# Optimization experiments

Hardware: AMD Instinct MI355X
Metric: run time of the kernel (lower is better)

## Reference

```python
import jax, jax.numpy as jnp
import numpy as np

N = 50000    # nodes
E = 600000   # edges
F = 128      # num_features
ED = 16      # edge_dim
H = 4        # heads
D = 32       # per-head channels = hidden_units // heads
HID = H * D  # hidden_units = 128
C = 10       # num_classes


def _lin(k, fan_in, fan_out):
    # torch.nn.Linear-style init scale
    return jax.random.uniform(k, (fan_in, fan_out), jnp.float32, -1.0, 1.0) / np.sqrt(fan_in)


def setup_inputs() -> dict:
    key = jax.random.key(0)
    ks = jax.random.split(key, 24)
    inp = {
        "x": jax.random.normal(ks[0], (N, F), jnp.float32),
        "edge_index": jax.random.randint(ks[1], (2, E), 0, N, dtype=jnp.int32),
        "edge_attr": jax.random.normal(ks[2], (E, ED), jnp.float32),
    }
    j = 3
    for l, ind in enumerate([F, HID]):
        specs = {"q": (ind, HID, True), "k": (ind, HID, True), "v": (ind, HID, True),
                 "e": (ED, HID, False), "s": (ind, HID, True)}
        for nm, (i, o, bias) in specs.items():
            inp[f"W{nm}{l}"] = _lin(ks[j], i, o); j += 1
            if bias:
                inp[f"b{nm}{l}"] = jnp.zeros((o,), jnp.float32)
    inp["Wout"] = _lin(ks[j], HID, C)
    inp["bout"] = jnp.zeros((C,), jnp.float32)
    return inp


def _transformer_conv(x, src, dst, eattr, Wq, bq, Wk, bk, Wv, bv, We, Ws, bs):
    # PyG TransformerConv: concat=True, root_weight=True, beta=False, eval dropout.
    n = x.shape[0]
    q = (x @ Wq + bq).reshape(n, H, D)
    k = (x @ Wk + bk).reshape(n, H, D)
    v = (x @ Wv + bv).reshape(n, H, D)
    e = (eattr @ We).reshape(-1, H, D)           # edge embedding, added to key and value
    kj = k[src] + e                              # [E, H, D]
    vj = v[src] + e                              # [E, H, D]
    logits = jnp.einsum("ehd,ehd->eh", q[dst], kj) / np.sqrt(D)
    m = jax.ops.segment_max(logits, dst, num_segments=n)          # [N, H]
    ex = jnp.exp(logits - m[dst])
    denom = jax.ops.segment_sum(ex, dst, num_segments=n)          # [N, H]
    alpha = ex / (denom[dst] + 1e-16)                             # PyG softmax eps
    out = jax.ops.segment_sum(vj * alpha[..., None], dst, num_segments=n)
    return out.reshape(n, HID) + x @ Ws + bs                      # concat heads + skip


def reference(x, edge_index, edge_attr,
              Wq0, bq0, Wk0, bk0, Wv0, bv0, We0, Ws0, bs0,
              Wq1, bq1, Wk1, bk1, Wv1, bv1, We1, Ws1, bs1,
              Wout, bout):
    src, dst = edge_index[0], edge_index[1]
    h = jax.nn.relu(_transformer_conv(x, src, dst, edge_attr,
                                      Wq0, bq0, Wk0, bk0, Wv0, bv0, We0, Ws0, bs0))
    h = jax.nn.relu(_transformer_conv(h, src, dst, edge_attr,
                                      Wq1, bq1, Wk1, bk1, Wv1, bv1, We1, Ws1, bs1))
    logits = h @ Wout + bout
    return jax.nn.log_softmax(logits, axis=1)
```

## Files before the change

kernel.cpp:

```cpp
#include <hip/hip_runtime.h>

typedef unsigned short u16;
typedef unsigned int u32;
typedef __attribute__((ext_vector_type(4))) u16 u16x4;
typedef __attribute__((ext_vector_type(8))) u16 u16x8;
typedef __attribute__((ext_vector_type(4))) u32 u32x4;
typedef __attribute__((ext_vector_type(8))) short short8;
typedef __attribute__((ext_vector_type(4))) float f32x4;
typedef __attribute__((ext_vector_type(4))) float f4;
typedef __attribute__((ext_vector_type(2))) float f2;

#define NN 50000
#define NE 600000
#define HEADS 4
#define DH 32
#define HIDU 128
#define NC 10
#define NBLK 196
#define WES_T 34
#define WES_H 546

#define SCALE2 0.25503486164f

__device__ __forceinline__ float bf2f(u16 u) {
    union { unsigned int i; float f; } c; c.i = ((unsigned int)u) << 16; return c.f;
}
__device__ __forceinline__ u16 f2bf(float f) {
    union { float f; unsigned int i; } c; c.f = f;
    unsigned int x = c.i;
    return (u16)((x + 0x7fffu + ((x >> 16) & 1u)) >> 16);
}
__device__ __forceinline__ float lo_bf(u32 d) { return __uint_as_float(d << 16); }
__device__ __forceinline__ float hi_bf(u32 d) { return __uint_as_float(d & 0xffff0000u); }
__device__ __forceinline__ float qadd_xor1(float v) {
    int o = __builtin_amdgcn_update_dpp(0, __float_as_int(v), 0xB1, 0xF, 0xF, true);
    return v + __int_as_float(o);
}
__device__ __forceinline__ float qadd_xor2(float v) {
    int o = __builtin_amdgcn_update_dpp(0, __float_as_int(v), 0x4E, 0xF, 0xF, true);
    return v + __int_as_float(o);
}

__global__ void k_zero(int* p, int n) {
    int i = blockIdx.x * blockDim.x + threadIdx.x;
    if (i < n) p[i] = 0;
}

__global__ void k_hist(const int* __restrict__ dst, int* __restrict__ deg) {
    int i = blockIdx.x * blockDim.x + threadIdx.x;
    if (i < NE) atomicAdd(&deg[dst[i]], 1);
}

__global__ __launch_bounds__(256) void scan_a(const int* __restrict__ deg,
                                              int* __restrict__ bsum) {
    __shared__ int red[4];
    int i = blockIdx.x * 256 + threadIdx.x;
    int v = (i < NN) ? deg[i] : 0;
    #pragma unroll
    for (int off = 1; off < 64; off <<= 1) v += __shfl_xor(v, off);
    if ((threadIdx.x & 63) == 0) red[threadIdx.x >> 6] = v;
    __syncthreads();
    if (threadIdx.x == 0) bsum[blockIdx.x] = red[0] + red[1] + red[2] + red[3];
}

__global__ __launch_bounds__(256) void scan_b(const int* __restrict__ bsum,
                                              int* __restrict__ boff,
                                              int* __restrict__ row_ptr) {
    __shared__ int s[256];
    int t = threadIdx.x;
    int v = (t < NBLK) ? bsum[t] : 0;
    s[t] = v;
    __syncthreads();
    for (int off = 1; off < 256; off <<= 1) {
        int x = (t >= off) ? s[t - off] : 0;
        __syncthreads();
        s[t] += x;
        __syncthreads();
    }
    if (t < NBLK) boff[t] = s[t] - v;
    if (t == 0) row_ptr[NN] = NE;
}

__global__ __launch_bounds__(256) void scan_c(const int* __restrict__ deg,
                                              const int* __restrict__ boff,
                                              int* __restrict__ row_ptr,
                                              int* __restrict__ cursor) {
    __shared__ int s[256];
    int t = threadIdx.x;
    int i = blockIdx.x * 256 + t;
    int v = (i < NN) ? deg[i] : 0;
    s[t] = v;
    __syncthreads();
    for (int off = 1; off < 256; off <<= 1) {
        int x = (t >= off) ? s[t - off] : 0;
        __syncthreads();
        s[t] += x;
        __syncthreads();
    }
    if (i < NN) {
        int r = boff[blockIdx.x] + s[t] - v;
        row_ptr[i] = r;
        cursor[i] = r;
    }
}

__global__ void k_scatter(const int* __restrict__ ei, const float* __restrict__ eattr,
                          int* __restrict__ cursor,
                          int* __restrict__ csr_src, u16* __restrict__ ea16) {
    int i = blockIdx.x * blockDim.x + threadIdx.x;
    if (i < NE) {
        int s = ei[i];
        int d = ei[NE + i];
        int pos = atomicAdd(&cursor[d], 1);
        csr_src[pos] = s;
        const f4* ep = (const f4*)(eattr + (size_t)i * 16);
        f4 a = ep[0], b = ep[1], c = ep[2], dd = ep[3];
        u16x8 o0, o1;
        #pragma unroll
        for (int j = 0; j < 4; j++) {
            o0[j] = f2bf(a[j]); o0[4 + j] = f2bf(b[j]);
            o1[j] = f2bf(c[j]); o1[4 + j] = f2bf(dd[j]);
        }
        *(u16x8*)(ea16 + (size_t)pos * 16)     = o0;
        *(u16x8*)(ea16 + (size_t)pos * 16 + 8) = o1;
    }
}

__global__ void k_cvtw(const float* w0, const float* w1, const float* w2, const float* w3,
                       const float* w4, const float* w5, const float* w6, const float* w7,
                       u16* __restrict__ hi) {
    const float* w;
    switch (blockIdx.x) {
        case 0: w = w0; break; case 1: w = w1; break;
        case 2: w = w2; break; case 3: w = w3; break;
        case 4: w = w4; break; case 5: w = w5; break;
        case 6: w = w6; break; default: w = w7; break;
    }
    u16* oh = hi + blockIdx.x * 16384;
    for (int i = 0; i < 64; i++) {
        int idx = threadIdx.x + i * 256;
        int k = idx >> 7, n = idx & 127;
        oh[n * 128 + k] = f2bf(w[idx]);
    }
}

__global__ __launch_bounds__(256) void gemm_qkvs(
    const float* __restrict__ X, const u16* __restrict__ WtHi,
    const float* __restrict__ b0, const float* __restrict__ b1,
    const float* __restrict__ b2, const float* __restrict__ b3,
    float* __restrict__ outq, u16* __restrict__ outk, u16* __restrict__ outv,
    float* __restrict__ outs, int nrows)
{
    __shared__ u16 Bs[128 * 128];
    const int mat = blockIdx.y;
    const u16* wh = WtHi + mat * 16384;

    #pragma unroll
    for (int i = 0; i < 8; i++) {
        int idx = threadIdx.x + i * 256;
        int n = idx >> 4, g = idx & 15;
        *(u16x8*)(&Bs[n * 128 + ((g ^ (n & 15)) << 3)]) = *(const u16x8*)(wh + n * 128 + g * 8);
    }
    __syncthreads();

    const int wave = threadIdx.x >> 6, lane = threadIdx.x & 63;
    const int n0 = lane & 15;
    const int qw = lane >> 4;
    const int kq = qw * 8;

    const float* xp[2];
    #pragma unroll
    for (int rt = 0; rt < 2; rt++) {
        int arow = blockIdx.x * 128 + wave * 32 + rt * 16 + n0;
        int arow_c = arow < nrows ? arow : nrows - 1;
        xp[rt] = X + (size_t)arow_c * HIDU + kq;
    }

    f32x4 acc[2][8];
    #pragma unroll
    for (int rt = 0; rt < 2; rt++)
        #pragma unroll
        for (int nt = 0; nt < 8; nt++) acc[rt][nt] = (f32x4){0.f, 0.f, 0.f, 0.f};

    #pragma unroll
    for (int ks = 0; ks < 4; ks++) {
        short8 ah[2];
        #pragma unroll
        for (int rt = 0; rt < 2; rt++) {
            f4 a0 = *(const f4*)(xp[rt] + ks * 32);
            f4 a1 = *(const f4*)(xp[rt] + ks * 32 + 4);
            #pragma unroll
            for (int j = 0; j < 4; j++) {
                ah[rt][j]     = (short)(__float_as_uint(a0[j]) >> 16);
                ah[rt][4 + j] = (short)(__float_as_uint(a1[j]) >> 16);
            }
        }
        #pragma unroll
        for (int nt = 0; nt < 8; nt++) {
            const int boff = (nt * 16 + n0) * 128 + (((ks << 2) + qw) ^ n0) * 8;
            short8 bh = *(const short8*)(&Bs[boff]);
            #pragma unroll
            for (int rt = 0; rt < 2; rt++)
                acc[rt][nt] = __builtin_amdgcn_mfma_f32_16x16x32_bf16(ah[rt], bh, acc[rt][nt], 0, 0, 0);
        }
    }

    const float* bia = (mat == 0) ? b0 : (mat == 1) ? b1 : (mat == 2) ? b2 : b3;
    #pragma unroll
    for (int rt = 0; rt < 2; rt++) {
        const int rbase = blockIdx.x * 128 + wave * 32 + rt * 16 + qw * 4;
        #pragma unroll
        for (int nt = 0; nt < 8; nt++) {
            int col = nt * 16 + n0;
            float bv = bia[col];
            #pragma unroll
            for (int r = 0; r < 4; r++) {
                int grow = rbase + r;
                if (grow < nrows) {
                    float v = acc[rt][nt][r] + bv;
                    if (mat == 0)      outq[(size_t)grow * HIDU + col] = v;
                    else if (mat == 1) outk[(size_t)grow * HIDU + col] = f2bf(v);
                    else if (mat == 2) outv[(size_t)grow * HIDU + col] = f2bf(v);
                    else               outs[(size_t)grow * HIDU + col] = v;
                }
            }
        }
    }
}

template<int MODE>
__global__ __launch_bounds__(256) void attn_t(
    const float* __restrict__ qb, const u16* __restrict__ kb, const u16* __restrict__ vb,
    const float* __restrict__ sb, const u16* __restrict__ ea16, const float* __restrict__ We,
    const int* __restrict__ row_ptr, const int* __restrict__ csr_src,
    float* __restrict__ hout_f32,
    const float* __restrict__ Wout, const float* __restrict__ bout,
    float* __restrict__ out_logits)
{
    __shared__ float WeS[4 * WES_H];
    __shared__ float WoT[MODE ? (NC * HIDU) : 1];
    __shared__ float boS[MODE ? NC : 1];

    #pragma unroll
    for (int i = 0; i < 8; i++) {
        int idx = threadIdx.x + i * 256;
        int tt = idx >> 7, c = idx & 127;
        int h = c >> 5, j = c & 31;
        WeS[h * WES_H + tt * WES_T + j] = We[idx];
    }
    if (MODE == 1) {
        #pragma unroll
        for (int i = 0; i < 5; i++) {
            int idx = threadIdx.x + i * 256;
            if (idx < HIDU * NC) {
                int c = idx >> 7, ch = idx & 127;
                WoT[idx] = Wout[ch * NC + c];
            }
        }
        if (threadIdx.x < NC) boS[threadIdx.x] = bout[threadIdx.x];
    }
    __syncthreads();

    int gtid = blockIdx.x * 256 + threadIdx.x;
    int n   = gtid >> 4;
    int l16 = gtid & 15;
    int h   = l16 >> 2;
    int sub = l16 & 3;
    const int lane = threadIdx.x & 63;
    const float* WeH = &WeS[h * WES_H];
    const int j0  = sub * 8;
    const int ch0 = h * DH + j0;
    const int t0  = sub * 4;

    f4 qa, qbv;
    {
        const f4* qp = (const f4*)(qb + (size_t)n * HIDU + ch0);
        qa = qp[0]; qbv = qp[1];
    }

    f4 g4v;
    {
        float part[16];
        #pragma unroll
        for (int t = 0; t < 16; t++) {
            const f2* wp = (const f2*)(WeH + t * WES_T + j0);
            f2 w0 = wp[0], w1 = wp[1], w2 = wp[2], w3 = wp[3];
            part[t] = qa[0] * w0.x + qa[1] * w0.y + qa[2] * w1.x + qa[3] * w1.y
                    + qbv[0] * w2.x + qbv[1] * w2.y + qbv[2] * w3.x + qbv[3] * w3.y;
        }
        #pragma unroll
        for (int t = 0; t < 16; t++) { part[t] = qadd_xor1(part[t]); part[t] = qadd_xor2(part[t]); }
        g4v[0] = part[t0]; g4v[1] = part[t0 + 1]; g4v[2] = part[t0 + 2]; g4v[3] = part[t0 + 3];
    }

    float m = -INFINITY, l = 0.f;
    f4 O0 = {0.f, 0.f, 0.f, 0.f}, O1 = {0.f, 0.f, 0.f, 0.f};
    f4 a4 = {0.f, 0.f, 0.f, 0.f};

    const int r0 = row_ptr[n], r1 = row_ptr[n + 1];

    for (int e = r0; e < r1; e += 4) {
        const int e1 = (e + 1 < r1) ? e + 1 : e;
        const int e2 = (e + 2 < r1) ? e + 2 : e;
        const int e3 = (e + 3 < r1) ? e + 3 : e;
        int s0 = csr_src[e], s1 = csr_src[e1], s2 = csr_src[e2], s3 = csr_src[e3];
        u16x4 x0 = *(const u16x4*)(ea16 + (size_t)e  * 16 + t0);
        u16x4 x1 = *(const u16x4*)(ea16 + (size_t)e1 * 16 + t0);
        u16x4 x2 = *(const u16x4*)(ea16 + (size_t)e2 * 16 + t0);
        u16x4 x3 = *(const u16x4*)(ea16 + (size_t)e3 * 16 + t0);
        u32x4 k0 = *(const u32x4*)(kb + (size_t)s0 * HIDU + ch0);
        u32x4 k1 = *(const u32x4*)(kb + (size_t)s1 * HIDU + ch0);
        u32x4 k2 = *(const u32x4*)(kb + (size_t)s2 * HIDU + ch0);
        u32x4 k3 = *(const u32x4*)(kb + (size_t)s3 * HIDU + ch0);
        u32x4 v0 = *(const u32x4*)(vb + (size_t)s0 * HIDU + ch0);
        u32x4 v1 = *(const u32x4*)(vb + (size_t)s1 * HIDU + ch0);
        u32x4 v2 = *(const u32x4*)(vb + (size_t)s2 * HIDU + ch0);
        u32x4 v3 = *(const u32x4*)(vb + (size_t)s3 * HIDU + ch0);

        f4 ea0 = {bf2f(x0[0]), bf2f(x0[1]), bf2f(x0[2]), bf2f(x0[3])};
        f4 ea1 = {bf2f(x1[0]), bf2f(x1[1]), bf2f(x1[2]), bf2f(x1[3])};
        f4 ea2 = {bf2f(x2[0]), bf2f(x2[1]), bf2f(x2[2]), bf2f(x2[3])};
        f4 ea3 = {bf2f(x3[0]), bf2f(x3[1]), bf2f(x3[2]), bf2f(x3[3])};

        f4 ac0 = qa * (f4){lo_bf(k0[0]), hi_bf(k0[0]), lo_bf(k0[1]), hi_bf(k0[1])}
               + qbv * (f4){lo_bf(k0[2]), hi_bf(k0[2]), lo_bf(k0[3]), hi_bf(k0[3])}
               + g4v * ea0;
        f4 ac1 = qa * (f4){lo_bf(k1[0]), hi_bf(k1[0]), lo_bf(k1[1]), hi_bf(k1[1])}
               + qbv * (f4){lo_bf(k1[2]), hi_bf(k1[2]), lo_bf(k1[3]), hi_bf(k1[3])}
               + g4v * ea1;
        f4 ac2 = qa * (f4){lo_bf(k2[0]), hi_bf(k2[0]), lo_bf(k2[1]), hi_bf(k2[1])}
               + qbv * (f4){lo_bf(k2[2]), hi_bf(k2[2]), lo_bf(k2[3]), hi_bf(k2[3])}
               + g4v * ea2;
        f4 ac3 = qa * (f4){lo_bf(k3[0]), hi_bf(k3[0]), lo_bf(k3[1]), hi_bf(k3[1])}
               + qbv * (f4){lo_bf(k3[2]), hi_bf(k3[2]), lo_bf(k3[3]), hi_bf(k3[3])}
               + g4v * ea3;
        float d0 = (ac0[0] + ac0[1]) + (ac0[2] + ac0[3]);
        float d1 = (ac1[0] + ac1[1]) + (ac1[2] + ac1[3]);
        float d2 = (ac2[0] + ac2[1]) + (ac2[2] + ac2[3]);
        float d3 = (ac3[0] + ac3[1]) + (ac3[2] + ac3[3]);
        d0 = qadd_xor1(d0); d1 = qadd_xor1(d1); d2 = qadd_xor1(d2); d3 = qadd_xor1(d3);
        d0 = qadd_xor2(d0); d1 = qadd_xor2(d1); d2 = qadd_xor2(d2); d3 = qadd_xor2(d3);

        float lg0 = d0 * SCALE2;
        float lg1 = (e + 1 < r1) ? d1 * SCALE2 : -INFINITY;
        float lg2 = (e + 2 < r1) ? d2 * SCALE2 : -INFINITY;
        float lg3 = (e + 3 < r1) ? d3 * SCALE2 : -INFINITY;
        float pm = fmaxf(fmaxf(lg0, lg1), fmaxf(lg2, lg3));
        float mn = fmaxf(m, pm);
        float corr = exp2f(m - mn);
        float w0 = exp2f(lg0 - mn);
        float w1 = exp2f(lg1 - mn);
        float w2 = exp2f(lg2 - mn);
        float w3 = exp2f(lg3 - mn);
        l = l * corr + ((w0 + w1) + (w2 + w3));

        O0 = O0 * corr
           + (f4){lo_bf(v0[0]), hi_bf(v0[0]), lo_bf(v0[1]), hi_bf(v0[1])} * w0
           + (f4){lo_bf(v1[0]), hi_bf(v1[0]), lo_bf(v1[1]), hi_bf(v1[1])} * w1
           + (f4){lo_bf(v2[0]), hi_bf(v2[0]), lo_bf(v2[1]), hi_bf(v2[1])} * w2
           + (f4){lo_bf(v3[0]), hi_bf(v3[0]), lo_bf(v3[1]), hi_bf(v3[1])} * w3;
        O1 = O1 * corr
           + (f4){lo_bf(v0[2]), hi_bf(v0[2]), lo_bf(v0[3]), hi_bf(v0[3])} * w0
           + (f4){lo_bf(v1[2]), hi_bf(v1[2]), lo_bf(v1[3]), hi_bf(v1[3])} * w1
           + (f4){lo_bf(v2[2]), hi_bf(v2[2]), lo_bf(v2[3]), hi_bf(v2[3])} * w2
           + (f4){lo_bf(v3[2]), hi_bf(v3[2]), lo_bf(v3[3]), hi_bf(v3[3])} * w3;
        a4 = a4 * corr + ea0 * w0 + ea1 * w1 + ea2 * w2 + ea3 * w3;
        m = mn;
    }

    float af[16];
    #pragma unroll
    for (int t = 0; t < 16; t++)
        af[t] = __shfl(a4[t & 3], (lane & ~3) | (t >> 2));

    float invl = 1.0f / (l + 1e-16f);
    const float* sp = sb + (size_t)n * HIDU + ch0;

    f4 evA = {0.f, 0.f, 0.f, 0.f}, evB = {0.f, 0.f, 0.f, 0.f};
    #pragma unroll
    for (int t = 0; t < 16; t++) {
        float a = af[t];
        const f2* wp = (const f2*)(WeH + t * WES_T + j0);
        f2 w0 = wp[0], w1 = wp[1], w2 = wp[2], w3 = wp[3];
        evA[0] += a * w0.x; evA[1] += a * w0.y; evA[2] += a * w1.x; evA[3] += a * w1.y;
        evB[0] += a * w2.x; evB[1] += a * w2.y; evB[2] += a * w3.x; evB[3] += a * w3.y;
    }

    f4 val0, val1;
    #pragma unroll
    for (int j = 0; j < 4; j++) {
        val0[j] = fmaxf((O0[j] + evA[j]) * invl + sp[j], 0.f);
        val1[j] = fmaxf((O1[j] + evB[j]) * invl + sp[4 + j], 0.f);
    }

    if (MODE == 0) {
        const size_t obase = (size_t)n * HIDU + ch0;
        *(f4*)(hout_f32 + obase) = val0;
        *(f4*)(hout_f32 + obase + 4) = val1;
    } else {
        float plg[NC];
        #pragma unroll
        for (int c = 0; c < NC; c++) {
            const f4* wr = (const f4*)(WoT + c * HIDU + ch0);
            f4 wa = wr[0], wb = wr[1];
            plg[c] = val0[0] * wa[0] + val0[1] * wa[1] + val0[2] * wa[2] + val0[3] * wa[3]
                   + val1[0] * wb[0] + val1[1] * wb[1] + val1[2] * wb[2] + val1[3] * wb[3];
        }
        #pragma unroll
        for (int mask = 1; mask < 16; mask <<= 1) {
            #pragma unroll
            for (int c = 0; c < NC; c++) plg[c] += __shfl_xor(plg[c], mask);
        }
        float lg[NC];
        float mx = -INFINITY;
        #pragma unroll
        for (int c = 0; c < NC; c++) { lg[c] = plg[c] + boS[c]; mx = fmaxf(mx, lg[c]); }
        float sum = 0.f;
        #pragma unroll
        for (int c = 0; c < NC; c++) sum += __expf(lg[c] - mx);
        float lse = mx + __logf(sum);
        if (l16 < NC) out_logits[(size_t)n * NC + l16] = lg[l16] - lse;
    }
}

extern "C" void kernel_launch(void* const* d_in, const int* in_sizes, int n_in,
                              void* d_out, int out_size, void* d_ws, size_t ws_size,
                              hipStream_t stream) {
    const float* x     = (const float*)d_in[0];
    const int*   ei    = (const int*)d_in[1];
    const float* eattr = (const float*)d_in[2];
    const float *Wq0 = (const float*)d_in[3],  *bq0 = (const float*)d_in[4];
    const float *Wk0 = (const float*)d_in[5],  *bk0 = (const float*)d_in[6];
    const float *Wv0 = (const float*)d_in[7],  *bv0 = (const float*)d_in[8];
    const float *We0 = (const float*)d_in[9];
    const float *Ws0 = (const float*)d_in[10], *bs0 = (const float*)d_in[11];
    const float *Wq1 = (const float*)d_in[12], *bq1 = (const float*)d_in[13];
    const float *Wk1 = (const float*)d_in[14], *bk1 = (const float*)d_in[15];
    const float *Wv1 = (const float*)d_in[16], *bv1 = (const float*)d_in[17];
    const float *We1 = (const float*)d_in[18];
    const float *Ws1 = (const float*)d_in[19], *bs1 = (const float*)d_in[20];
    const float *Wout = (const float*)d_in[21], *bout = (const float*)d_in[22];

    char* p = (char*)d_ws;
    auto alloc = [&](size_t bytes) -> void* {
        void* r = (void*)p;
        p += (bytes + 255) & ~(size_t)255;
        return r;
    };
    int* deg      = (int*)alloc(NN * 4);
    int* row_ptr  = (int*)alloc((NN + 1) * 4);
    int* cursor   = (int*)alloc(NN * 4);
    int* bsum     = (int*)alloc(NBLK * 4);
    int* boff     = (int*)alloc(NBLK * 4);
    int* csr_src  = (int*)alloc((size_t)NE * 4);
    float* qb     = (float*)alloc((size_t)NN * HIDU * 4);
    u16* kb       = (u16*)alloc((size_t)NN * HIDU * 2);
    u16* vb       = (u16*)alloc((size_t)NN * HIDU * 2);
    float* sbuf   = (float*)alloc((size_t)NN * HIDU * 4);
    float* hbuf   = (float*)alloc((size_t)NN * HIDU * 4);
    u16* ea16     = (u16*)alloc((size_t)NE * 16 * 2);
    u16* wthi     = (u16*)alloc(8 * 16384 * 2);

    k_zero<<<(NN + 255) / 256, 256, 0, stream>>>(deg, NN);
    k_hist<<<(NE + 255) / 256, 256, 0, stream>>>(ei + NE, deg);
    scan_a<<<NBLK, 256, 0, stream>>>(deg, bsum);
    scan_b<<<1, 256, 0, stream>>>(bsum, boff, row_ptr);
    scan_c<<<NBLK, 256, 0, stream>>>(deg, boff, row_ptr, cursor);
    k_scatter<<<(NE + 255) / 256, 256, 0, stream>>>(ei, eattr, cursor, csr_src, ea16);

    k_cvtw<<<8, 256, 0, stream>>>(Wq0, Wk0, Wv0, Ws0, Wq1, Wk1, Wv1, Ws1, wthi);

    const int gm = (NN + 127) / 128;
    const int ga = (NN * 16) / 256;

    gemm_qkvs<<<dim3(gm, 4), 256, 0, stream>>>(x, wthi, bq0, bk0, bv0, bs0,
                                               qb, kb, vb, sbuf, NN);
    attn_t<0><<<ga, 256, 0, stream>>>(qb, kb, vb, sbuf, ea16, We0, row_ptr, csr_src,
                                      hbuf, nullptr, nullptr, nullptr);
    gemm_qkvs<<<dim3(gm, 4), 256, 0, stream>>>(hbuf, wthi + 4 * 16384, bq1, bk1, bv1, bs1,
                                               qb, kb, vb, sbuf, NN);
    attn_t<1><<<ga, 256, 0, stream>>>(qb, kb, vb, sbuf, ea16, We1, row_ptr, csr_src,
                                      nullptr, Wout, bout, (float*)d_out);
}
```

Baseline: 433.1 us.

## Prefetch next edge batch, drop online-softmax max, parallelize weight conversion

The attention loop now software-prefetches the next four edges' source indices and edge attributes one iteration ahead, using padding appended to the CSR arrays so reads past the end stay in bounds. It removes the running-max rescaling of online softmax and accumulates plain exp2 weights, which cuts the per-edge correction multiplies and max reductions but risks overflow if logits grow large. Weight conversion is spread over an 8x8 grid instead of 8 blocks, and the skip-term reads are vectorized.

```diff
diff --git a/kernel.cpp b/kernel.cpp
--- a/kernel.cpp
+++ b/kernel.cpp
@@ -65,7 +65,9 @@
 
 __global__ __launch_bounds__(256) void scan_b(const int* __restrict__ bsum,
                                               int* __restrict__ boff,
-                                              int* __restrict__ row_ptr) {
+                                              int* __restrict__ row_ptr,
+                                              int* __restrict__ csr_src,
+                                              u16* __restrict__ ea16) {
     __shared__ int s[256];
     int t = threadIdx.x;
     int v = (t < NBLK) ? bsum[t] : 0;
@@ -79,6 +81,8 @@
     }
     if (t < NBLK) boff[t] = s[t] - v;
     if (t == 0) row_ptr[NN] = NE;
+    if (t < 8)  csr_src[NE + t] = 0;
+    if (t < 128) ea16[(size_t)NE * 16 + t] = 0;
 }
 
 __global__ __launch_bounds__(256) void scan_c(const int* __restrict__ deg,
@@ -137,8 +141,9 @@
         case 6: w = w6; break; default: w = w7; break;
     }
     u16* oh = hi + blockIdx.x * 16384;
-    for (int i = 0; i < 64; i++) {
-        int idx = threadIdx.x + i * 256;
+    #pragma unroll
+    for (int i = 0; i < 8; i++) {
+        int idx = threadIdx.x + (blockIdx.y * 8 + i) * 256;
         int k = idx >> 7, n = idx & 127;
         oh[n * 128 + k] = f2bf(w[idx]);
     }
@@ -293,21 +298,24 @@
         g4v[0] = part[t0]; g4v[1] = part[t0 + 1]; g4v[2] = part[t0 + 2]; g4v[3] = part[t0 + 3];
     }
 
-    float m = -INFINITY, l = 0.f;
+    float l = 0.f;
     f4 O0 = {0.f, 0.f, 0.f, 0.f}, O1 = {0.f, 0.f, 0.f, 0.f};
     f4 a4 = {0.f, 0.f, 0.f, 0.f};
 
     const int r0 = row_ptr[n], r1 = row_ptr[n + 1];
 
+    int s0 = 0, s1 = 0, s2 = 0, s3 = 0;
+    u16x4 x0 = {0,0,0,0}, x1 = {0,0,0,0}, x2 = {0,0,0,0}, x3 = {0,0,0,0};
+    if (r0 < r1) {
+        s0 = csr_src[r0];     s1 = csr_src[r0 + 1];
+        s2 = csr_src[r0 + 2]; s3 = csr_src[r0 + 3];
+        x0 = *(const u16x4*)(ea16 + (size_t)r0 * 16 + t0);
+        x1 = *(const u16x4*)(ea16 + (size_t)(r0 + 1) * 16 + t0);
+        x2 = *(const u16x4*)(ea16 + (size_t)(r0 + 2) * 16 + t0);
+        x3 = *(const u16x4*)(ea16 + (size_t)(r0 + 3) * 16 + t0);
+    }
+
     for (int e = r0; e < r1; e += 4) {
-        const int e1 = (e + 1 < r1) ? e + 1 : e;
-        const int e2 = (e + 2 < r1) ? e + 2 : e;
-        const int e3 = (e + 3 < r1) ? e + 3 : e;
-        int s0 = csr_src[e], s1 = csr_src[e1], s2 = csr_src[e2], s3 = csr_src[e3];
-        u16x4 x0 = *(const u16x4*)(ea16 + (size_t)e  * 16 + t0);
-        u16x4 x1 = *(const u16x4*)(ea16 + (size_t)e1 * 16 + t0);
-        u16x4 x2 = *(const u16x4*)(ea16 + (size_t)e2 * 16 + t0);
-        u16x4 x3 = *(const u16x4*)(ea16 + (size_t)e3 * 16 + t0);
         u32x4 k0 = *(const u32x4*)(kb + (size_t)s0 * HIDU + ch0);
         u32x4 k1 = *(const u32x4*)(kb + (size_t)s1 * HIDU + ch0);
         u32x4 k2 = *(const u32x4*)(kb + (size_t)s2 * HIDU + ch0);
@@ -316,6 +324,12 @@
         u32x4 v1 = *(const u32x4*)(vb + (size_t)s1 * HIDU + ch0);
         u32x4 v2 = *(const u32x4*)(vb + (size_t)s2 * HIDU + ch0);
         u32x4 v3 = *(const u32x4*)(vb + (size_t)s3 * HIDU + ch0);
+        int ns0 = csr_src[e + 4], ns1 = csr_src[e + 5];
+        int ns2 = csr_src[e + 6], ns3 = csr_src[e + 7];
+        u16x4 nx0 = *(const u16x4*)(ea16 + (size_t)(e + 4) * 16 + t0);
+        u16x4 nx1 = *(const u16x4*)(ea16 + (size_t)(e + 5) * 16 + t0);
+        u16x4 nx2 = *(const u16x4*)(ea16 + (size_t)(e + 6) * 16 + t0);
+        u16x4 nx3 = *(const u16x4*)(ea16 + (size_t)(e + 7) * 16 + t0);
 
         f4 ea0 = {bf2f(x0[0]), bf2f(x0[1]), bf2f(x0[2]), bf2f(x0[3])};
         f4 ea1 = {bf2f(x1[0]), bf2f(x1[1]), bf2f(x1[2]), bf2f(x1[3])};
@@ -341,31 +355,26 @@
         d0 = qadd_xor1(d0); d1 = qadd_xor1(d1); d2 = qadd_xor1(d2); d3 = qadd_xor1(d3);
         d0 = qadd_xor2(d0); d1 = qadd_xor2(d1); d2 = qadd_xor2(d2); d3 = qadd_xor2(d3);
 
-        float lg0 = d0 * SCALE2;
-        float lg1 = (e + 1 < r1) ? d1 * SCALE2 : -INFINITY;
-        float lg2 = (e + 2 < r1) ? d2 * SCALE2 : -INFINITY;
-        float lg3 = (e + 3 < r1) ? d3 * SCALE2 : -INFINITY;
-        float pm = fmaxf(fmaxf(lg0, lg1), fmaxf(lg2, lg3));
-        float mn = fmaxf(m, pm);
-        float corr = exp2f(m - mn);
-        float w0 = exp2f(lg0 - mn);
-        float w1 = exp2f(lg1 - mn);
-        float w2 = exp2f(lg2 - mn);
-        float w3 = exp2f(lg3 - mn);
-        l = l * corr + ((w0 + w1) + (w2 + w3));
-
-        O0 = O0 * corr
+        float w0 = exp2f(d0 * SCALE2);
+        float w1 = (e + 1 < r1) ? exp2f(d1 * SCALE2) : 0.f;
+        float w2 = (e + 2 < r1) ? exp2f(d2 * SCALE2) : 0.f;
+        float w3 = (e + 3 < r1) ? exp2f(d3 * SCALE2) : 0.f;
+        l += (w0 + w1) + (w2 + w3);
+
+        O0 = O0
            + (f4){lo_bf(v0[0]), hi_bf(v0[0]), lo_bf(v0[1]), hi_bf(v0[1])} * w0
            + (f4){lo_bf(v1[0]), hi_bf(v1[0]), lo_bf(v1[1]), hi_bf(v1[1])} * w1
            + (f4){lo_bf(v2[0]), hi_bf(v2[0]), lo_bf(v2[1]), hi_bf(v2[1])} * w2
            + (f4){lo_bf(v3[0]), hi_bf(v3[0]), lo_bf(v3[1]), hi_bf(v3[1])} * w3;
-        O1 = O1 * corr
+        O1 = O1
            + (f4){lo_bf(v0[2]), hi_bf(v0[2]), lo_bf(v0[3]), hi_bf(v0[3])} * w0
            + (f4){lo_bf(v1[2]), hi_bf(v1[2]), lo_bf(v1[3]), hi_bf(v1[3])} * w1
            + (f4){lo_bf(v2[2]), hi_bf(v2[2]), lo_bf(v2[3]), hi_bf(v2[3])} * w2
            + (f4){lo_bf(v3[2]), hi_bf(v3[2]), lo_bf(v3[3]), hi_bf(v3[3])} * w3;
-        a4 = a4 * corr + ea0 * w0 + ea1 * w1 + ea2 * w2 + ea3 * w3;
-        m = mn;
+        a4 = a4 + ea0 * w0 + ea1 * w1 + ea2 * w2 + ea3 * w3;
+
+        s0 = ns0; s1 = ns1; s2 = ns2; s3 = ns3;
+        x0 = nx0; x1 = nx1; x2 = nx2; x3 = nx3;
     }
 
     float af[16];
@@ -374,7 +383,8 @@
         af[t] = __shfl(a4[t & 3], (lane & ~3) | (t >> 2));
 
     float invl = 1.0f / (l + 1e-16f);
-    const float* sp = sb + (size_t)n * HIDU + ch0;
+    const f4* sp = (const f4*)(sb + (size_t)n * HIDU + ch0);
+    f4 sp0 = sp[0], sp1 = sp[1];
 
     f4 evA = {0.f, 0.f, 0.f, 0.f}, evB = {0.f, 0.f, 0.f, 0.f};
     #pragma unroll
@@ -389,8 +399,8 @@
     f4 val0, val1;
     #pragma unroll
     for (int j = 0; j < 4; j++) {
-        val0[j] = fmaxf((O0[j] + evA[j]) * invl + sp[j], 0.f);
-        val1[j] = fmaxf((O1[j] + evB[j]) * invl + sp[4 + j], 0.f);
+        val0[j] = fmaxf((O0[j] + evA[j]) * invl + sp0[j], 0.f);
+        val1[j] = fmaxf((O1[j] + evB[j]) * invl + sp1[j], 0.f);
     }
 
     if (MODE == 0) {
@@ -452,23 +462,23 @@
     int* cursor   = (int*)alloc(NN * 4);
     int* bsum     = (int*)alloc(NBLK * 4);
     int* boff     = (int*)alloc(NBLK * 4);
-    int* csr_src  = (int*)alloc((size_t)NE * 4);
+    int* csr_src  = (int*)alloc(((size_t)NE + 8) * 4);
     float* qb     = (float*)alloc((size_t)NN * HIDU * 4);
     u16* kb       = (u16*)alloc((size_t)NN * HIDU * 2);
     u16* vb       = (u16*)alloc((size_t)NN * HIDU * 2);
     float* sbuf   = (float*)alloc((size_t)NN * HIDU * 4);
     float* hbuf   = (float*)alloc((size_t)NN * HIDU * 4);
-    u16* ea16     = (u16*)alloc((size_t)NE * 16 * 2);
+    u16* ea16     = (u16*)alloc(((size_t)NE + 8) * 16 * 2);
     u16* wthi     = (u16*)alloc(8 * 16384 * 2);
 
     k_zero<<<(NN + 255) / 256, 256, 0, stream>>>(deg, NN);
     k_hist<<<(NE + 255) / 256, 256, 0, stream>>>(ei + NE, deg);
     scan_a<<<NBLK, 256, 0, stream>>>(deg, bsum);
-    scan_b<<<1, 256, 0, stream>>>(bsum, boff, row_ptr);
+    scan_b<<<1, 256, 0, stream>>>(bsum, boff, row_ptr, csr_src, ea16);
     scan_c<<<NBLK, 256, 0, stream>>>(deg, boff, row_ptr, cursor);
     k_scatter<<<(NE + 255) / 256, 256, 0, stream>>>(ei, eattr, cursor, csr_src, ea16);
 
-    k_cvtw<<<8, 256, 0, stream>>>(Wq0, Wk0, Wv0, Ws0, Wq1, Wk1, Wv1, Ws1, wthi);
+    k_cvtw<<<dim3(8, 8), 256, 0, stream>>>(Wq0, Wk0, Wv0, Ws0, Wq1, Wk1, Wv1, Ws1, wthi);
 
     const int gm = (NN + 127) / 128;
     const int ga = (NN * 16) / 256;
```

Result: no change. 434.7 us (+0.4%).
